# Kernel tuning notes

Measured on AMD Instinct MI355X. Metric: run time of the kernel, lower is better.

## Reference

```python
import jax, jax.numpy as jnp
import numpy as np

N = 50000      # nodes
E = 800000     # edges
F = 64         # num_features
H = 64         # hidden_channels
L = 3          # num_layers
C0 = 16        # conv1d_channels[0]
TOTAL = H * L + 1  # 193, concat dim / Conv1d kernel size


def setup_inputs() -> dict:
    key = jax.random.key(0)
    ks = jax.random.split(key, 13)
    s = 0.05
    x = jax.random.normal(ks[0], (N, F), jnp.float32)
    edge_index = jax.random.randint(ks[1], (2, E), 0, N)
    edge_attr = jax.random.normal(ks[2], (E, 1), jnp.float32)
    W0 = jax.random.normal(ks[3], (F, H), jnp.float32) * s
    b0 = jnp.zeros((H,), jnp.float32)
    W1 = jax.random.normal(ks[4], (H, H), jnp.float32) * s
    b1 = jnp.zeros((H,), jnp.float32)
    W2 = jax.random.normal(ks[5], (H, H), jnp.float32) * s
    b2 = jnp.zeros((H,), jnp.float32)
    W3 = jax.random.normal(ks[6], (H, 1), jnp.float32) * s
    b3 = jnp.zeros((1,), jnp.float32)
    conv_w = jax.random.normal(ks[7], (C0, TOTAL), jnp.float32) * s  # Conv1d(1,C0,K=TOTAL,stride=TOTAL) weight squeezed
    conv_b = jnp.zeros((C0,), jnp.float32)
    return dict(x=x, edge_index=edge_index, edge_attr=edge_attr,
                W0=W0, b0=b0, W1=W1, b1=b1, W2=W2, b2=b2, W3=W3, b3=b3,
                conv_w=conv_w, conv_b=conv_b)


def _gcn(h, W, b, src, dst, norm):
    # PyG GCNConv: h' = segsum_dst(norm * (h W)[src]) + b
    h = h @ W                                   # [N, out]
    msg = h[src] * norm[:, None]                # [E+N, out] gather (irregular)
    out = jax.ops.segment_sum(msg, dst, num_segments=N)
    return out + b


def reference(x, edge_index, edge_attr, W0, b0, W1, b1, W2, b2, W3, b3, conv_w, conv_b):
    del edge_attr  # use_edge_attr=False
    loops = jnp.arange(N, dtype=edge_index.dtype)
    src = jnp.concatenate([edge_index[0], loops])  # add self-loops
    dst = jnp.concatenate([edge_index[1], loops])
    deg = jax.ops.segment_sum(jnp.ones_like(dst, dtype=x.dtype), dst, num_segments=N)
    dinv = jax.lax.rsqrt(jnp.maximum(deg, 1.0))
    norm = dinv[src] * dinv[dst]

    xs = []
    h = x
    for W, b in ((W0, b0), (W1, b1), (W2, b2), (W3, b3)):
        h = _gcn(h, W, b, src, dst, norm)
        xs.append(h)
    cat = jnp.concatenate(xs, axis=-1)           # [N, TOTAL] (k=1 drops input x)
    # Conv1d(1, C0, K=TOTAL, stride=TOTAL) over length-TOTAL signal == dense projection
    out = cat @ conv_w.T + conv_b                # [N, C0]
    return out
```

## Files before the change

kernel.cpp:

```cpp
#include <hip/hip_runtime.h>
#include <math.h>

static constexpr int N    = 50000;
static constexpr int E    = 800000;
static constexpr int TE   = E + N;
static constexpr int NC   = 16;
static constexpr int TOT  = 193;
static constexpr int NB   = (N + 255) / 256;

static constexpr int KQ1 = 0;
static constexpr int KQ2 = 1024;
static constexpr int KQ3 = 2048;
static constexpr int KV  = 3072;
static constexpr int KU1 = 3136;
static constexpr int KU2 = 3152;
static constexpr int KD  = 3168;
static constexpr int KSC = 3184;
static constexpr int KSZ = 3200;

__device__ __forceinline__ unsigned short f2bf(float f) {
    union { float f; unsigned int i; } v; v.f = f;
    unsigned int b = v.i + 0x7FFFu + ((v.i >> 16) & 1u);
    return (unsigned short)(b >> 16);
}


__global__ void k_count(const int* __restrict__ dst, int* __restrict__ deg,
                        int* __restrict__ pos) {
    int e = blockIdx.x * blockDim.x + threadIdx.x;
    if (e < E) pos[e] = atomicAdd(&deg[dst[e]], 1);
}

__global__ __launch_bounds__(256) void k_part(const int* __restrict__ deg,
                                              int* __restrict__ part) {
    __shared__ int red[256];
    const int t = threadIdx.x;
    int i = blockIdx.x * 256 + t;
    int v = (i < N) ? (deg[i] + 1) : 0;
    red[t] = v;
    __syncthreads();
#pragma unroll
    for (int off = 128; off; off >>= 1) {
        if (t < off) red[t] += red[t + off];
        __syncthreads();
    }
    if (t == 0) part[blockIdx.x] = red[0];
}

__global__ __launch_bounds__(256) void k_scanpart(int* __restrict__ part) {
    __shared__ int s[256];
    const int t = threadIdx.x;
    int v = (t < NB) ? part[t] : 0;
    s[t] = v;
    __syncthreads();
#pragma unroll
    for (int off = 1; off < 256; off <<= 1) {
        int u = (t >= off) ? s[t - off] : 0;
        __syncthreads();
        s[t] += u;
        __syncthreads();
    }
    if (t < NB) part[t] = s[t] - v;
}

__global__ __launch_bounds__(256) void k_scatter(const int* __restrict__ deg,
                                                 const int* __restrict__ part,
                                                 int* __restrict__ row_ptr,
                                                 float* __restrict__ dinv) {
    __shared__ int s[256];
    const int t = threadIdx.x;
    int i = blockIdx.x * 256 + t;
    int v = (i < N) ? (deg[i] + 1) : 0;
    s[t] = v;
    __syncthreads();
#pragma unroll
    for (int off = 1; off < 256; off <<= 1) {
        int u = (t >= off) ? s[t - off] : 0;
        __syncthreads();
        s[t] += u;
        __syncthreads();
    }
    if (i < N) {
        int base = part[blockIdx.x];
        row_ptr[i] = base + s[t] - v;
        dinv[i] = rsqrtf((float)v);
        if (i == N - 1) row_ptr[N] = base + s[t];
    }
}

__global__ void k_fill(const int* __restrict__ src, const int* __restrict__ dst,
                       const int* __restrict__ pos,
                       const int* __restrict__ row_ptr,
                       const float* __restrict__ dinv,
                       int2* __restrict__ edges) {
    int idx = blockIdx.x * blockDim.x + threadIdx.x;
    if (idx < E) {
        int s = src[idx], d = dst[idx];
        int p = row_ptr[d] + 1 + pos[idx];
        edges[p] = make_int2(s, __float_as_int(dinv[s] * dinv[d]));
    } else if (idx < TE) {
        int i = idx - E;
        float dv = dinv[i];
        edges[row_ptr[i]] = make_int2(i, __float_as_int(dv * dv));
    }
}

__global__ __launch_bounds__(256) void k_xbf(const float* __restrict__ x,
                                             ushort* __restrict__ xb) {
    int i = blockIdx.x * 256 + threadIdx.x;
    if (i * 4 >= N * 64) return;
    float4 v = ((const float4*)x)[i];
    ushort4 o;
    o.x = f2bf(v.x); o.y = f2bf(v.y); o.z = f2bf(v.z); o.w = f2bf(v.w);
    ((ushort4*)xb)[i] = o;
}

__global__ __launch_bounds__(256) void k_setup(
    const float* __restrict__ W0, const float* __restrict__ b0,
    const float* __restrict__ W1, const float* __restrict__ b1,
    const float* __restrict__ W2, const float* __restrict__ b2,
    const float* __restrict__ W3, const float* __restrict__ b3,
    const float* __restrict__ cw, const float* __restrict__ cb,
    float* __restrict__ K) {
    __shared__ float W0s[4096], W1s[4096], W2s[4096], P2s[4096];
    __shared__ float C1[1024], C2[1024], C3[1024], R3s[1024];
    __shared__ float W3s[64], b0s[64], b1s[64], b2s[64];
    __shared__ float r3[64], rb1[64], rb2[64], rb12[64];
    const int t = threadIdx.x;
    const int k = t >> 2, q = t & 3;

    for (int i = t; i < 4096; i += 256) {
        W0s[i] = W0[i]; W1s[i] = W1[i]; W2s[i] = W2[i];
    }
    for (int i = t; i < 1024; i += 256) {
        int j = i >> 4, c = i & 15;
        C1[i] = cw[c * TOT + j];
        C2[i] = cw[c * TOT + 64 + j];
        C3[i] = cw[c * TOT + 128 + j];
    }
    if (t < 64) { W3s[t] = W3[t]; b0s[t] = b0[t]; b1s[t] = b1[t]; b2s[t] = b2[t]; }
    __syncthreads();

    {
        const int j0 = q * 16;
        float acc[16];
#pragma unroll
        for (int jj = 0; jj < 16; ++jj) acc[jj] = 0.f;
        for (int m = 0; m < 64; ++m) {
            float w = W0s[k * 64 + m];
#pragma unroll
            for (int jj = 0; jj < 16; ++jj) acc[jj] += w * W1s[m * 64 + j0 + jj];
        }
#pragma unroll
        for (int jj = 0; jj < 16; ++jj) P2s[k * 64 + j0 + jj] = acc[jj];
    }
    {
        const int c0 = q * 4;
        float acc[4] = {0.f, 0.f, 0.f, 0.f};
        for (int j = 0; j < 64; ++j) {
            float w = W2s[k * 64 + j];
#pragma unroll
            for (int cc = 0; cc < 4; ++cc) acc[cc] += w * C3[j * 16 + c0 + cc];
        }
#pragma unroll
        for (int cc = 0; cc < 4; ++cc) R3s[k * 16 + c0 + cc] = acc[cc];
    }
    if (q == 0) {
        float a = 0.f;
        for (int j = 0; j < 64; ++j) a += W2s[k * 64 + j] * W3s[j];
        r3[k] = a;
    }
    if (q == 1) {
        float a = 0.f;
        for (int m = 0; m < 64; ++m) a += b0s[m] * W1s[m * 64 + k];
        rb1[k] = a;
    }
    if (q == 2) {
        float a = 0.f;
        for (int m = 0; m < 64; ++m) a += b1s[m] * W2s[m * 64 + k];
        rb2[k] = a;
    }
    __syncthreads();

    {
        const int c0 = q * 4;
        float q1[4] = {0,0,0,0}, q2[4] = {0,0,0,0}, q3[4] = {0,0,0,0};
        for (int j = 0; j < 64; ++j) {
            float w0 = W0s[k * 64 + j], p2 = P2s[k * 64 + j];
#pragma unroll
            for (int cc = 0; cc < 4; ++cc) {
                q1[cc] += w0 * C1[j * 16 + c0 + cc];
                q2[cc] += p2 * C2[j * 16 + c0 + cc];
                q3[cc] += p2 * R3s[j * 16 + c0 + cc];
            }
        }
#pragma unroll
        for (int cc = 0; cc < 4; ++cc) {
            K[KQ1 + k * 16 + c0 + cc] = q1[cc];
            K[KQ2 + k * 16 + c0 + cc] = q2[cc];
            K[KQ3 + k * 16 + c0 + cc] = q3[cc];
        }
    }
    if (q == 3) {
        float a = 0.f;
        for (int j = 0; j < 64; ++j) a += P2s[k * 64 + j] * r3[j];
        K[KV + k] = a;
    }
    if (q == 0) {
        float a = 0.f;
        for (int m = 0; m < 64; ++m) a += rb1[m] * W2s[m * 64 + k];
        rb12[k] = a;
    }
    __syncthreads();

    if (t < 16) {
        float a1 = 0.f, a2 = 0.f, ad = 0.f;
        for (int j = 0; j < 64; ++j) {
            a1 += rb1[j] * C2[j * 16 + t] + rb2[j] * C3[j * 16 + t];
            a2 += rb12[j] * C3[j * 16 + t];
            ad += b0s[j] * C1[j * 16 + t] + b1s[j] * C2[j * 16 + t]
                + b2s[j] * C3[j * 16 + t];
        }
        K[KU1 + t] = a1; K[KU2 + t] = a2; K[KD + t] = ad + cb[t];
    }
    if (t == 0) {
        float al = 0.f, be = 0.f, ga = 0.f;
        for (int j = 0; j < 64; ++j) {
            al += rb12[j] * W3s[j]; be += rb2[j] * W3s[j]; ga += b2s[j] * W3s[j];
        }
        K[KSC + 0] = al; K[KSC + 1] = be; K[KSC + 2] = ga;
    }
}

template <int LAYER>
__global__ __launch_bounds__(256) void k_layer(
    const ushort* __restrict__ Min,
    const int2* __restrict__ edges,
    const int* __restrict__ row_ptr,
    const float* __restrict__ K,
    const float* __restrict__ s1in,
    const float* __restrict__ s2in,
    ushort* __restrict__ Mout,
    float* __restrict__ s_out,
    float* __restrict__ t4,
    float* __restrict__ out) {
    __shared__ float QT[64 * 17];
    const int tid = threadIdx.x;
    constexpr int KQ = (LAYER == 0) ? KQ1 : (LAYER == 1) ? KQ2 : KQ3;
    for (int i = tid; i < 1024; i += 256) {
        int j = i >> 4, c = i & 15;
        QT[j * 17 + c] = K[KQ + i];
    }
    const int lane = tid & 63;
    const int w    = tid >> 6;
    const int half = lane >> 5;
    const int m    = lane & 31;
    float vlo = 0.f, vhi = 0.f;
    if constexpr (LAYER == 2) { vlo = K[KV + 2 * m]; vhi = K[KV + 2 * m + 1]; }
    __syncthreads();

    const int nn = blockIdx.x * 8 + w * 2 + half;
    const int rp0 = row_ptr[nn], rp1 = row_ptr[nn + 1];
    const int d = rp1 - rp0;
    int dmax = max(d, __shfl_xor(d, 32));
    const int trips = __builtin_amdgcn_readfirstlane((dmax + 7) >> 3);

    float acc_lo = 0.f, acc_hi = 0.f, accs = 0.f;
    for (int t = 0; t < trips; ++t) {
        const int base = rp0 + t * 8;
        int col[8]; float wv[8];
#pragma unroll
        for (int i = 0; i < 8; ++i) {
            int pi = base + i;
            int pc = min(pi, rp1 - 1);
            int2 e = edges[pc];
            col[i] = e.x;
            wv[i] = (pi < rp1) ? __int_as_float(e.y) : 0.f;
        }
        unsigned int g[8];
#pragma unroll
        for (int i = 0; i < 8; ++i)
            g[i] = *(const unsigned int*)(Min + col[i] * 64 + 2 * m);
        if constexpr (LAYER == 0) {
#pragma unroll
            for (int i = 0; i < 8; ++i) accs += wv[i];
        }
#pragma unroll
        for (int i = 0; i < 8; ++i) {
            union { unsigned int u; float f; } flo, fhi;
            flo.u = g[i] << 16;
            fhi.u = g[i] & 0xFFFF0000u;
            acc_lo += wv[i] * flo.f;
            acc_hi += wv[i] * fhi.f;
        }
    }

    if constexpr (LAYER < 2) {
        unsigned int pk = (unsigned int)f2bf(acc_lo)
                        | ((unsigned int)f2bf(acc_hi) << 16);
        ((unsigned int*)Mout)[nn * 32 + m] = pk;
    }
    if constexpr (LAYER == 0) {
        if (m == 0) s_out[nn] = accs;
    }
    if constexpr (LAYER == 1) {
        float ss = 0.f;
        for (int p = rp0 + m; p < rp1; p += 32) {
            int2 e = edges[p];
            ss += __int_as_float(e.y) * s1in[e.x];
        }
#pragma unroll
        for (int off = 16; off; off >>= 1) ss += __shfl_xor(ss, off);
        if (m == 0) s_out[nn] = ss;
    }

    float s1n = 0.f, s2n = 0.f;
    if constexpr (LAYER == 2) {
        s1n = s1in[nn]; s2n = s2in[nn];
        float tv = acc_lo * vlo + acc_hi * vhi;
#pragma unroll
        for (int off = 16; off; off >>= 1) tv += __shfl_xor(tv, off);
        if (m == 0)
            t4[nn] = tv + K[KSC + 0] * s2n + K[KSC + 1] * s1n + K[KSC + 2];
    }

    const int c = m & 15, gq = m >> 4;
    float r = 0.f;
#pragma unroll
    for (int i = 0; i < 32; ++i) {
        int srcl = (half << 5) + (gq << 4) + (i >> 1);
        float aj = __shfl((i & 1) ? acc_hi : acc_lo, srcl);
        r += aj * QT[((gq << 5) + i) * 17 + c];
    }
    r += __shfl_xor(r, 16);
    if (m < 16) {
        int o = nn * NC + c;
        if constexpr (LAYER == 0) {
            out[o] = K[KD + c] + r;
        } else if constexpr (LAYER == 1) {
            out[o] += r;
        } else {
            out[o] += r + s1n * K[KU1 + c] + s2n * K[KU2 + c];
        }
    }
}

__global__ __launch_bounds__(256) void k_agg4_out(
    const float* __restrict__ t4, const int2* __restrict__ edges,
    const int* __restrict__ row_ptr, const float* __restrict__ b3,
    const float* __restrict__ conv_w, float* __restrict__ out) {
    int n = blockIdx.x * blockDim.x + threadIdx.x;
    if (n >= N) return;
    int p0 = row_ptr[n], p1 = row_ptr[n + 1];
    float a0 = 0.f, a1 = 0.f;
    for (int p = p0; p < p1; p += 4) {
        int q0 = min(p, p1 - 1), q1 = min(p + 1, p1 - 1);
        int q2 = min(p + 2, p1 - 1), q3 = min(p + 3, p1 - 1);
        int2 e0 = edges[q0], e1 = edges[q1], e2 = edges[q2], e3 = edges[q3];
        float w0 = __int_as_float(e0.y);
        float w1 = (p + 1 < p1) ? __int_as_float(e1.y) : 0.f;
        float w2 = (p + 2 < p1) ? __int_as_float(e2.y) : 0.f;
        float w3 = (p + 3 < p1) ? __int_as_float(e3.y) : 0.f;
        a0 += w0 * t4[e0.x]; a1 += w1 * t4[e1.x];
        a0 += w2 * t4[e2.x]; a1 += w3 * t4[e3.x];
    }
    float h4 = a0 + a1 + b3[0];
    float4* o4 = (float4*)(out + n * NC);
#pragma unroll
    for (int k = 0; k < 4; ++k) {
        float4 v = o4[k];
        v.x += h4 * conv_w[(4 * k + 0) * TOT + 192];
        v.y += h4 * conv_w[(4 * k + 1) * TOT + 192];
        v.z += h4 * conv_w[(4 * k + 2) * TOT + 192];
        v.w += h4 * conv_w[(4 * k + 3) * TOT + 192];
        o4[k] = v;
    }
}


extern "C" void kernel_launch(void* const* d_in, const int* in_sizes, int n_in,
                              void* d_out, int out_size, void* d_ws, size_t ws_size,
                              hipStream_t stream) {
    const float* x   = (const float*)d_in[0];
    const int*   ei  = (const int*)d_in[1];
    const int*   src = ei;
    const int*   dst = ei + E;
    const float* W0  = (const float*)d_in[3];
    const float* b0  = (const float*)d_in[4];
    const float* W1  = (const float*)d_in[5];
    const float* b1  = (const float*)d_in[6];
    const float* W2  = (const float*)d_in[7];
    const float* b2  = (const float*)d_in[8];
    const float* W3  = (const float*)d_in[9];
    const float* b3  = (const float*)d_in[10];
    const float* cw  = (const float*)d_in[11];
    const float* cb  = (const float*)d_in[12];
    float* out = (float*)d_out;

    char* p = (char*)d_ws;
    auto alloc = [&](size_t nbytes) {
        char* r = p;
        p += (nbytes + 255) & ~(size_t)255;
        return (void*)r;
    };
    int*    deg     = (int*)alloc((size_t)N * 4);
    int*    pos     = (int*)alloc((size_t)E * 4);
    int*    row_ptr = (int*)alloc((size_t)(N + 1) * 4);
    float*  dinv    = (float*)alloc((size_t)N * 4);
    int*    part    = (int*)alloc((size_t)NB * 4);
    int2*   edges   = (int2*)alloc((size_t)TE * 8);
    ushort* xb      = (ushort*)alloc((size_t)N * 64 * 2);
    ushort* M1      = (ushort*)alloc((size_t)N * 64 * 2);
    ushort* M2      = (ushort*)alloc((size_t)N * 64 * 2);
    float*  s1      = (float*)alloc((size_t)N * 4);
    float*  s2      = (float*)alloc((size_t)N * 4);
    float*  t4      = (float*)alloc((size_t)N * 4);
    float*  K       = (float*)alloc((size_t)KSZ * 4);

    k_setup<<<1, 256, 0, stream>>>(W0, b0, W1, b1, W2, b2, W3, b3, cw, cb, K);
    k_xbf<<<(N * 64 / 4 + 255) / 256, 256, 0, stream>>>(x, xb);

    hipMemsetAsync(deg, 0, (size_t)N * 4, stream);
    k_count   <<<(E + 255) / 256, 256, 0, stream>>>(dst, deg, pos);
    k_part    <<<NB, 256, 0, stream>>>(deg, part);
    k_scanpart<<<1, 256, 0, stream>>>(part);
    k_scatter <<<NB, 256, 0, stream>>>(deg, part, row_ptr, dinv);
    k_fill    <<<(TE + 255) / 256, 256, 0, stream>>>(src, dst, pos, row_ptr, dinv, edges);

    const int layerGrid = N / 8;

    k_layer<0><<<layerGrid, 256, 0, stream>>>(
        xb, edges, row_ptr, K, nullptr, nullptr, M1, s1, nullptr, out);
    k_layer<1><<<layerGrid, 256, 0, stream>>>(
        M1, edges, row_ptr, K, s1, nullptr, M2, s2, nullptr, out);
    k_layer<2><<<layerGrid, 256, 0, stream>>>(
        M2, edges, row_ptr, K, s1, s2, nullptr, nullptr, t4, out);
    k_agg4_out<<<(N + 255) / 256, 256, 0, stream>>>(t4, edges, row_ptr, b3, cw, out);
}
```

Before: 192.7 us.

## Pad degree counters per cache line and process four nodes per wavefront

Degree counters are spread 16 ints apart so each node's atomic sits on its own 64-byte line, which is meant to reduce contention between neighbouring counters. Each counting thread now handles two edges. The layer kernel assigns 16 lanes per node, each loading 8 bytes (four bf16 features), so one wavefront covers four nodes and issues fewer, wider gathers. The trade-offs are a 16x larger memset and degree array read with a stride, plus more divergence from taking the max degree over four nodes instead of two.

After: 177.9 us. 1.08x faster.

```diff
diff --git a/kernel.cpp b/kernel.cpp
--- a/kernel.cpp
+++ b/kernel.cpp
@@ -7,6 +7,7 @@
 static constexpr int NC   = 16;
 static constexpr int TOT  = 193;
 static constexpr int NB   = (N + 255) / 256;
+static constexpr int DP   = 16;
 
 static constexpr int KQ1 = 0;
 static constexpr int KQ2 = 1024;
@@ -25,18 +26,24 @@
 }
 
 
-__global__ void k_count(const int* __restrict__ dst, int* __restrict__ deg,
+__global__ void k_count(const int* __restrict__ dst, int* __restrict__ degp,
                         int* __restrict__ pos) {
     int e = blockIdx.x * blockDim.x + threadIdx.x;
-    if (e < E) pos[e] = atomicAdd(&deg[dst[e]], 1);
-}
-
-__global__ __launch_bounds__(256) void k_part(const int* __restrict__ deg,
+    if (e < E / 2) {
+        int d0 = dst[e], d1 = dst[e + E / 2];
+        int p0 = atomicAdd(&degp[d0 * DP], 1);
+        int p1 = atomicAdd(&degp[d1 * DP], 1);
+        pos[e] = p0;
+        pos[e + E / 2] = p1;
+    }
+}
+
+__global__ __launch_bounds__(256) void k_part(const int* __restrict__ degp,
                                               int* __restrict__ part) {
     __shared__ int red[256];
     const int t = threadIdx.x;
     int i = blockIdx.x * 256 + t;
-    int v = (i < N) ? (deg[i] + 1) : 0;
+    int v = (i < N) ? (degp[i * DP] + 1) : 0;
     red[t] = v;
     __syncthreads();
 #pragma unroll
@@ -63,14 +70,14 @@
     if (t < NB) part[t] = s[t] - v;
 }
 
-__global__ __launch_bounds__(256) void k_scatter(const int* __restrict__ deg,
+__global__ __launch_bounds__(256) void k_scatter(const int* __restrict__ degp,
                                                  const int* __restrict__ part,
                                                  int* __restrict__ row_ptr,
                                                  float* __restrict__ dinv) {
     __shared__ int s[256];
     const int t = threadIdx.x;
     int i = blockIdx.x * 256 + t;
-    int v = (i < N) ? (deg[i] + 1) : 0;
+    int v = (i < N) ? (degp[i * DP] + 1) : 0;
     s[t] = v;
     __syncthreads();
 #pragma unroll
@@ -253,19 +260,23 @@
     }
     const int lane = tid & 63;
     const int w    = tid >> 6;
-    const int half = lane >> 5;
-    const int m    = lane & 31;
-    float vlo = 0.f, vhi = 0.f;
-    if constexpr (LAYER == 2) { vlo = K[KV + 2 * m]; vhi = K[KV + 2 * m + 1]; }
-    __syncthreads();
-
-    const int nn = blockIdx.x * 8 + w * 2 + half;
+    const int q    = lane >> 4;
+    const int m    = lane & 15;
+    float v0 = 0.f, v1 = 0.f, v2 = 0.f, v3 = 0.f;
+    if constexpr (LAYER == 2) {
+        v0 = K[KV + 4 * m + 0]; v1 = K[KV + 4 * m + 1];
+        v2 = K[KV + 4 * m + 2]; v3 = K[KV + 4 * m + 3];
+    }
+    __syncthreads();
+
+    const int nn = blockIdx.x * 16 + w * 4 + q;
     const int rp0 = row_ptr[nn], rp1 = row_ptr[nn + 1];
     const int d = rp1 - rp0;
-    int dmax = max(d, __shfl_xor(d, 32));
+    int dmax = max(d, __shfl_xor(d, 16));
+    dmax = max(dmax, __shfl_xor(dmax, 32));
     const int trips = __builtin_amdgcn_readfirstlane((dmax + 7) >> 3);
 
-    float acc_lo = 0.f, acc_hi = 0.f, accs = 0.f;
+    float a0 = 0.f, a1 = 0.f, a2 = 0.f, a3 = 0.f, accs = 0.f;
     for (int t = 0; t < trips; ++t) {
         const int base = rp0 + t * 8;
         int col[8]; float wv[8];
@@ -277,70 +288,75 @@
             col[i] = e.x;
             wv[i] = (pi < rp1) ? __int_as_float(e.y) : 0.f;
         }
-        unsigned int g[8];
+        unsigned long long g[8];
 #pragma unroll
         for (int i = 0; i < 8; ++i)
-            g[i] = *(const unsigned int*)(Min + col[i] * 64 + 2 * m);
+            g[i] = *(const unsigned long long*)(Min + col[i] * 64 + 4 * m);
         if constexpr (LAYER == 0) {
 #pragma unroll
             for (int i = 0; i < 8; ++i) accs += wv[i];
         }
 #pragma unroll
         for (int i = 0; i < 8; ++i) {
-            union { unsigned int u; float f; } flo, fhi;
-            flo.u = g[i] << 16;
-            fhi.u = g[i] & 0xFFFF0000u;
-            acc_lo += wv[i] * flo.f;
-            acc_hi += wv[i] * fhi.f;
+            unsigned int lo = (unsigned int)g[i];
+            unsigned int hi = (unsigned int)(g[i] >> 32);
+            union { unsigned int u; float f; } x0, x1, x2, x3;
+            x0.u = lo << 16; x1.u = lo & 0xFFFF0000u;
+            x2.u = hi << 16; x3.u = hi & 0xFFFF0000u;
+            a0 += wv[i] * x0.f; a1 += wv[i] * x1.f;
+            a2 += wv[i] * x2.f; a3 += wv[i] * x3.f;
         }
     }
 
     if constexpr (LAYER < 2) {
-        unsigned int pk = (unsigned int)f2bf(acc_lo)
-                        | ((unsigned int)f2bf(acc_hi) << 16);
-        ((unsigned int*)Mout)[nn * 32 + m] = pk;
+        unsigned long long pk =
+              (unsigned long long)f2bf(a0)
+            | ((unsigned long long)f2bf(a1) << 16)
+            | ((unsigned long long)f2bf(a2) << 32)
+            | ((unsigned long long)f2bf(a3) << 48);
+        ((unsigned long long*)Mout)[nn * 16 + m] = pk;
     }
     if constexpr (LAYER == 0) {
         if (m == 0) s_out[nn] = accs;
     }
     if constexpr (LAYER == 1) {
         float ss = 0.f;
-        for (int p = rp0 + m; p < rp1; p += 32) {
+        for (int p = rp0 + m; p < rp1; p += 16) {
             int2 e = edges[p];
             ss += __int_as_float(e.y) * s1in[e.x];
         }
-#pragma unroll
-        for (int off = 16; off; off >>= 1) ss += __shfl_xor(ss, off);
+        ss += __shfl_xor(ss, 1); ss += __shfl_xor(ss, 2);
+        ss += __shfl_xor(ss, 4); ss += __shfl_xor(ss, 8);
         if (m == 0) s_out[nn] = ss;
     }
 
     float s1n = 0.f, s2n = 0.f;
     if constexpr (LAYER == 2) {
         s1n = s1in[nn]; s2n = s2in[nn];
-        float tv = acc_lo * vlo + acc_hi * vhi;
-#pragma unroll
-        for (int off = 16; off; off >>= 1) tv += __shfl_xor(tv, off);
+        float tv = a0 * v0 + a1 * v1 + a2 * v2 + a3 * v3;
+        tv += __shfl_xor(tv, 1); tv += __shfl_xor(tv, 2);
+        tv += __shfl_xor(tv, 4); tv += __shfl_xor(tv, 8);
         if (m == 0)
             t4[nn] = tv + K[KSC + 0] * s2n + K[KSC + 1] * s1n + K[KSC + 2];
     }
 
-    const int c = m & 15, gq = m >> 4;
     float r = 0.f;
 #pragma unroll
-    for (int i = 0; i < 32; ++i) {
-        int srcl = (half << 5) + (gq << 4) + (i >> 1);
-        float aj = __shfl((i & 1) ? acc_hi : acc_lo, srcl);
-        r += aj * QT[((gq << 5) + i) * 17 + c];
-    }
-    r += __shfl_xor(r, 16);
-    if (m < 16) {
-        int o = nn * NC + c;
+    for (int a = 0; a < 16; ++a) {
+        int srcl = (q << 4) + a;
+        float f0 = __shfl(a0, srcl), f1 = __shfl(a1, srcl);
+        float f2 = __shfl(a2, srcl), f3 = __shfl(a3, srcl);
+        r += f0 * QT[(4 * a + 0) * 17 + m] + f1 * QT[(4 * a + 1) * 17 + m]
+           + f2 * QT[(4 * a + 2) * 17 + m] + f3 * QT[(4 * a + 3) * 17 + m];
+    }
+    {
+        int o = nn * NC + m;
         if constexpr (LAYER == 0) {
-            out[o] = K[KD + c] + r;
+            out[o] = K[KD + m] + r;
         } else if constexpr (LAYER == 1) {
             out[o] += r;
         } else {
-            out[o] += r + s1n * K[KU1 + c] + s2n * K[KU2 + c];
+            out[o] += r + s1n * K[KU1 + m] + s2n * K[KU2 + m];
         }
     }
 }
@@ -403,7 +419,7 @@
         p += (nbytes + 255) & ~(size_t)255;
         return (void*)r;
     };
-    int*    deg     = (int*)alloc((size_t)N * 4);
+    int*    degp    = (int*)alloc((size_t)N * DP * 4);
     int*    pos     = (int*)alloc((size_t)E * 4);
     int*    row_ptr = (int*)alloc((size_t)(N + 1) * 4);
     float*  dinv    = (float*)alloc((size_t)N * 4);
@@ -420,14 +436,14 @@
     k_setup<<<1, 256, 0, stream>>>(W0, b0, W1, b1, W2, b2, W3, b3, cw, cb, K);
     k_xbf<<<(N * 64 / 4 + 255) / 256, 256, 0, stream>>>(x, xb);
 
-    hipMemsetAsync(deg, 0, (size_t)N * 4, stream);
-    k_count   <<<(E + 255) / 256, 256, 0, stream>>>(dst, deg, pos);
-    k_part    <<<NB, 256, 0, stream>>>(deg, part);
+    hipMemsetAsync(degp, 0, (size_t)N * DP * 4, stream);
+    k_count   <<<(E / 2 + 255) / 256, 256, 0, stream>>>(dst, degp, pos);
+    k_part    <<<NB, 256, 0, stream>>>(degp, part);
     k_scanpart<<<1, 256, 0, stream>>>(part);
-    k_scatter <<<NB, 256, 0, stream>>>(deg, part, row_ptr, dinv);
+    k_scatter <<<NB, 256, 0, stream>>>(degp, part, row_ptr, dinv);
     k_fill    <<<(TE + 255) / 256, 256, 0, stream>>>(src, dst, pos, row_ptr, dinv, edges);
 
-    const int layerGrid = N / 8;
+    const int layerGrid = N / 16;
 
     k_layer<0><<<layerGrid, 256, 0, stream>>>(
         xb, edges, row_ptr, K, nullptr, nullptr, M1, s1, nullptr, out);
```
